# Optimization experiments

Measured on AMD Instinct MI355X. Metric: run time of the kernel, lower is better.

The kernel has to match this reference:

```python
import jax, jax.numpy as jnp
import numpy as np
import math

HEAD_DIM = 128
THETA = 10000.0
MASK_VAL = -10000.0


def _rope(x, cos, sin):
    # x: (B, S, D); cos/sin: (S, D//2). Pairs (even, odd) rotated as complex.
    xr = x.reshape(*x.shape[:-1], -1, 2)
    xe, xo = xr[..., 0], xr[..., 1]
    oe = xe * cos - xo * sin
    oo = xe * sin + xo * cos
    return jnp.stack([oe, oo], axis=-1).reshape(x.shape)


def setup_inputs() -> dict:
    key = jax.random.key(0)
    B, S, D = 8, 4096, HEAD_DIM
    qkv = jax.random.normal(key, (B, S, 3 * D), dtype=jnp.float32)
    return {"qkv": qkv}


def reference(qkv):
    B, S, threeD = qkv.shape
    D = threeD // 3
    qkv = qkv.reshape(B, S, 3, D)
    q, k, v = qkv[:, :, 0], qkv[:, :, 1], qkv[:, :, 2]

    # precompute_freqs_cis: outer(t, 1/theta^(2i/d)) -> cos/sin (S, D//2)
    inv_freq = 1.0 / (THETA ** (jnp.arange(0, D, 2, dtype=jnp.float32) / D))
    freqs = jnp.arange(S, dtype=jnp.float32)[:, None] * inv_freq[None, :]
    cos, sin = jnp.cos(freqs), jnp.sin(freqs)
    q = _rope(q, cos, sin)
    k = _rope(k, cos, sin)

    scale = 1.0 / math.sqrt(D)
    scores = jnp.einsum('btd,bsd->bts', q, k) * scale  # (B, S, S)
    causal_mask = jnp.triu(jnp.full((S, S), MASK_VAL, dtype=scores.dtype), 1)
    attn = jax.nn.softmax(scores + causal_mask, axis=-1)
    out = jnp.einsum('bts,bsd->btd', attn, v)  # (B, S, D)
    return out
```

## Files before the change

kernel.cpp:

```cpp
#include <hip/hip_runtime.h>
#include <math.h>

typedef _Float16 half8 __attribute__((ext_vector_type(8)));
typedef float floatx4 __attribute__((ext_vector_type(4)));
typedef float floatx2 __attribute__((ext_vector_type(2)));

#define B_ 8
#define S_ 4096
#define SCALE_L2E 0.12751743008389106f
#define MASK_L2E  -14426.950408889634f
#define L2_10K_OVER_128 0.10381025296522975f

#define PLD2 40
#define KW  136
#define VW  24
#define OSTLD 136
#define SLOTS_PER_B 576
#define NW 8
#define POOL_HALFS (16384 + NW * 2 * 16 * PLD2)

__device__ __forceinline__ int chunk_prefix(int qt32) {
    int g = qt32 >> 4;
    return qt32 + 8 * g * (g - 1) + (qt32 - (g << 4)) * g;
}

__device__ __forceinline__ void glds16(const _Float16* src, _Float16* dst) {
    __builtin_amdgcn_global_load_lds((const __attribute__((address_space(1))) void*)src,
                                     (__attribute__((address_space(3))) void*)dst, 16, 0, 0);
}

__global__ __launch_bounds__(256) void prep_kernel(const float* __restrict__ qkv,
                                                   _Float16* __restrict__ Qh,
                                                   _Float16* __restrict__ Kp,
                                                   _Float16* __restrict__ Vp) {
    __shared__ __align__(16) _Float16 Kl[16][KW];
    __shared__ __align__(16) _Float16 Vt[128][VW];
    const int tid = threadIdx.x;
    const int b   = blockIdx.y;
    const int s0  = blockIdx.x * 16;

#pragma unroll
    for (int it = 0; it < 4; ++it) {
        int idx = tid + it * 256;
        int i = idx & 63, sr = idx >> 6, s = s0 + sr;
        const float* base = qkv + ((size_t)(b * S_ + s)) * 384 + 2 * i;
        floatx2 q2 = *(const floatx2*)base;
        floatx2 k2 = *(const floatx2*)(base + 128);
        float inv = exp2f(-(float)(2 * i) * L2_10K_OVER_128);
        float ang = (float)s * inv;
        float sn, cs;
        __sincosf(ang, &sn, &cs);
        size_t oq = ((size_t)(b * S_ + s)) * 128 + 2 * i;
        Qh[oq]     = (_Float16)((q2[0] * cs - q2[1] * sn) * SCALE_L2E);
        Qh[oq + 1] = (_Float16)((q2[0] * sn + q2[1] * cs) * SCALE_L2E);
        Kl[sr][2 * i]     = (_Float16)(k2[0] * cs - k2[1] * sn);
        Kl[sr][2 * i + 1] = (_Float16)(k2[0] * sn + k2[1] * cs);
    }
#pragma unroll
    for (int it = 0; it < 2; ++it) {
        int idx = tid + it * 256;
        int c = idx & 31, sr = idx >> 5;
        floatx4 v = *(const floatx4*)(qkv + ((size_t)(b * S_ + s0 + sr)) * 384 + 256 + c * 4);
#pragma unroll
        for (int j = 0; j < 4; ++j) Vt[c * 4 + j][sr] = (_Float16)v[j];
    }
    __syncthreads();

    {
        int c = tid >> 6, lane = tid & 63;
        int quad = lane >> 4, n = lane & 15;
        half8 val = *(const half8*)&Kl[n][c * 32 + quad * 8];
        int s16 = s0 >> 4;
        *(half8*)(Kp + (((size_t)(b * 256 + s16) * 4 + c) * 64 + lane) * 8) = val;
    }
    {
        int kt = s0 >> 6, c2 = (s0 >> 5) & 1, qp = (s0 >> 4) & 1;
        int nt = tid >> 5, lq = (tid >> 4) & 1, n = tid & 15;
        int quad = qp * 2 + lq;
        int lane = quad * 16 + n;
        half8 val = *(const half8*)&Vt[nt * 16 + n][lq * 8];
        *(half8*)(Vp + ((((size_t)(b * 64 + kt) * 2 + c2) * 8 + nt) * 64 + lane) * 8) = val;
    }
}

__global__ __launch_bounds__(512) void attn_part_kernel(const _Float16* __restrict__ Qh,
                                                        const _Float16* __restrict__ Kp,
                                                        const _Float16* __restrict__ Vp,
                                                        _Float16* __restrict__ Ppart,
                                                        float* __restrict__ Lpart) {
    __shared__ __align__(16) _Float16 POOL[POOL_HALFS];

    const int tid  = threadIdx.x;
    const int w    = tid >> 6;
    const int lane = tid & 63;
    const int quad = lane >> 4;
    const int l16  = lane & 15;
    const int b     = blockIdx.x & 7;
    const int chunk = blockIdx.x >> 3;
    const int c0    = chunk * 8;

    const int qt32_top  = 127 - blockIdx.y * 8;
    const int ktmax_blk = (qt32_top * 32 + 31) >> 6;
    if (c0 > ktmax_blk) return;
    const int kend_blk  = min(ktmax_blk, c0 + 7);

    const int qt32   = qt32_top - w;
    const int qr0    = qt32 * 32;
    const int kt_max = (qr0 + 31) >> 6;
    const bool has_work = (c0 <= kt_max);
    const int kend   = min(kt_max, c0 + 7);
    const int slot   = b * SLOTS_PER_B + chunk_prefix(qt32) + chunk;
    _Float16* Pw = POOL + 16384 + w * (2 * 16 * PLD2);

    half8 aq[2][4];
#pragma unroll
    for (int tile = 0; tile < 2; ++tile) {
        const _Float16* Qb = Qh + ((size_t)(b * S_) + qr0 + tile * 16 + l16) * 128;
#pragma unroll
        for (int c = 0; c < 4; ++c) aq[tile][c] = *(const half8*)(Qb + c * 32 + quad * 8);
    }

    floatx4 o[2][8];
#pragma unroll
    for (int tile = 0; tile < 2; ++tile)
#pragma unroll
        for (int i = 0; i < 8; ++i) o[tile][i] = (floatx4){0.f, 0.f, 0.f, 0.f};
    float rsum[2][4] = {{0.f, 0.f, 0.f, 0.f}, {0.f, 0.f, 0.f, 0.f}};

    const _Float16* Kb = Kp + (size_t)b * 524288;
    const _Float16* Vb = Vp + (size_t)b * 524288;

    const int ht0    = 2 * c0;
    const int ht_end = 2 * kend_blk + 1;

    {
        const _Float16* ks = Kb + (size_t)ht0 * 4096 + w * 512 + lane * 8;
        const _Float16* vs = Vb + (size_t)ht0 * 4096 + w * 512 + lane * 8;
        glds16(ks, POOL + w * 512);
        glds16(vs, POOL + 4096 + w * 512);
    }

    for (int ht = ht0; ht <= ht_end; ++ht) {
        const int buf = ht & 1;
        if (ht < ht_end) {
            const _Float16* ks = Kb + (size_t)(ht + 1) * 4096 + w * 512 + lane * 8;
            const _Float16* vs = Vb + (size_t)(ht + 1) * 4096 + w * 512 + lane * 8;
            _Float16* kd = POOL + (buf ^ 1) * 8192 + w * 512;
            glds16(ks, kd);
            glds16(vs, kd + 4096);
            asm volatile("s_waitcnt vmcnt(2)" ::: "memory");
        } else {
            asm volatile("s_waitcnt vmcnt(0)" ::: "memory");
        }
        __builtin_amdgcn_s_barrier();

        const int kt = ht >> 1, h = ht & 1;
        if (has_work && kt <= kend) {
            const _Float16* Klds = POOL + buf * 8192;
            const _Float16* Vlds = Klds + 4096;

            floatx4 s4[2][2];
#pragma unroll
            for (int tl = 0; tl < 2; ++tl) {
                half8 bk[4];
#pragma unroll
                for (int c = 0; c < 4; ++c)
                    bk[c] = *(const half8*)&Klds[((tl * 4 + c) * 64 + lane) * 8];
                floatx4 a0 = (floatx4){0.f, 0.f, 0.f, 0.f};
                floatx4 a1 = (floatx4){0.f, 0.f, 0.f, 0.f};
                __builtin_amdgcn_s_setprio(1);
#pragma unroll
                for (int c = 0; c < 4; ++c) {
                    a0 = __builtin_amdgcn_mfma_f32_16x16x32_f16(aq[0][c], bk[c], a0, 0, 0, 0);
                    a1 = __builtin_amdgcn_mfma_f32_16x16x32_f16(aq[1][c], bk[c], a1, 0, 0, 0);
                }
                __builtin_amdgcn_s_setprio(0);
                s4[0][tl] = a0; s4[1][tl] = a1;
            }

            if (kt == kt_max) {
#pragma unroll
                for (int tile = 0; tile < 2; ++tile)
#pragma unroll
                    for (int tl = 0; tl < 2; ++tl)
#pragma unroll
                        for (int r = 0; r < 4; ++r) {
                            int kcol = kt * 64 + h * 32 + tl * 16 + l16;
                            int qr   = qr0 + tile * 16 + quad * 4 + r;
                            if (kcol > qr) s4[tile][tl][r] += MASK_L2E;
                        }
            }

#pragma unroll
            for (int tile = 0; tile < 2; ++tile)
#pragma unroll
                for (int tl = 0; tl < 2; ++tl)
#pragma unroll
                    for (int r = 0; r < 4; ++r) {
                        float p = __builtin_amdgcn_exp2f(s4[tile][tl][r]);
                        rsum[tile][r] += p;
                        Pw[tile * (16 * PLD2) + (quad * 4 + r) * PLD2 + tl * 16 + l16] = (_Float16)p;
                    }

            {
                half8 vf[8];
#pragma unroll
                for (int nt = 0; nt < 8; ++nt)
                    vf[nt] = *(const half8*)&Vlds[(nt * 64 + lane) * 8];
#pragma unroll
                for (int tile = 0; tile < 2; ++tile) {
                    half8 ap = *(const half8*)&Pw[tile * (16 * PLD2) + l16 * PLD2 + quad * 8];
                    __builtin_amdgcn_s_setprio(1);
#pragma unroll
                    for (int nt = 0; nt < 8; ++nt)
                        o[tile][nt] = __builtin_amdgcn_mfma_f32_16x16x32_f16(ap, vf[nt], o[tile][nt], 0, 0, 0);
                    __builtin_amdgcn_s_setprio(0);
                }
            }
        }
        asm volatile("" ::: "memory");
        __builtin_amdgcn_s_barrier();
    }

    if (!has_work) return;

#pragma unroll
    for (int off = 1; off <= 8; off <<= 1)
#pragma unroll
        for (int tile = 0; tile < 2; ++tile)
#pragma unroll
            for (int r = 0; r < 4; ++r)
                rsum[tile][r] += __shfl_xor(rsum[tile][r], off, 64);
    if (l16 == 0) {
#pragma unroll
        for (int tile = 0; tile < 2; ++tile)
#pragma unroll
            for (int r = 0; r < 4; ++r)
                Lpart[(size_t)slot * 32 + tile * 16 + quad * 4 + r] = rsum[tile][r];
    }

    asm volatile("" ::: "memory");
    _Float16* Ost = POOL + w * (POOL_HALFS / NW);
    _Float16* pp = Ppart + (size_t)slot * 4096;
#pragma unroll
    for (int tile = 0; tile < 2; ++tile) {
#pragma unroll
        for (int nt = 0; nt < 8; ++nt)
#pragma unroll
            for (int r = 0; r < 4; ++r)
                Ost[(quad * 4 + r) * OSTLD + nt * 16 + l16] = (_Float16)o[tile][nt][r];
#pragma unroll
        for (int i = 0; i < 4; ++i) {
            int idx = lane + i * 64;
            half8 v = *(const half8*)&Ost[(idx >> 4) * OSTLD + (idx & 15) * 8];
            *(half8*)(pp + ((size_t)tile * 256 + idx) * 8) = v;
        }
    }
}

__global__ __launch_bounds__(256) void reduce_kernel(const _Float16* __restrict__ Ppart,
                                                     const float* __restrict__ Lpart,
                                                     float* __restrict__ out) {
    const int bid  = blockIdx.x;
    const int b    = bid >> 7;
    const int qt32 = bid & 127;
    const int qr0  = qt32 * 32;
    const int nch  = (((qr0 + 31) >> 6) >> 3) + 1;
    const int slot0 = b * SLOTS_PER_B + chunk_prefix(qt32);
    const _Float16* pp = Ppart + (size_t)slot0 * 4096;
    const float* lp = Lpart + (size_t)slot0 * 32;
    const int tid = threadIdx.x;

#pragma unroll
    for (int j = 0; j < 2; ++j) {
        int idx = tid + j * 256;
        int row = idx >> 4;
        float acc[8] = {0.f, 0.f, 0.f, 0.f, 0.f, 0.f, 0.f, 0.f};
        float l = 0.f;
        for (int c = 0; c < nch; ++c) {
            half8 v = *(const half8*)(pp + (size_t)c * 4096 + (size_t)idx * 8);
#pragma unroll
            for (int k = 0; k < 8; ++k) acc[k] += (float)v[k];
            l += lp[c * 32 + row];
        }
        float inv = 1.0f / l;
        float* ob = out + ((size_t)(b * S_) + qr0) * 128 + (size_t)idx * 8;
        floatx4 o0 = (floatx4){acc[0] * inv, acc[1] * inv, acc[2] * inv, acc[3] * inv};
        floatx4 o1 = (floatx4){acc[4] * inv, acc[5] * inv, acc[6] * inv, acc[7] * inv};
        *(floatx4*)ob = o0;
        *(floatx4*)(ob + 4) = o1;
    }
}

#define PLD 72
__global__ __launch_bounds__(64) void attn_atomic_kernel(const _Float16* __restrict__ Qh,
                                                         const _Float16* __restrict__ Kp,
                                                         const _Float16* __restrict__ Vp,
                                                         float* __restrict__ out,
                                                         float* __restrict__ Lg) {
    __shared__ __align__(16) _Float16 Pl[2][16 * PLD];
    const int lane = threadIdx.x, quad = lane >> 4, l16 = lane & 15;
    const int b = blockIdx.x & 7, chunk = blockIdx.x >> 3;
    const int qt = 255 - blockIdx.y, qr0 = qt * 16;
    const int kt_max = qt >> 2, c0 = chunk * 8;
    if (c0 > kt_max) return;
    const int kend = min(kt_max, c0 + 7);
    const _Float16* Qb = Qh + ((size_t)(b * S_) + qr0 + l16) * 128;
    half8 aq[4];
#pragma unroll
    for (int c = 0; c < 4; ++c) aq[c] = *(const half8*)(Qb + c * 32 + quad * 8);
    floatx4 o[8];
#pragma unroll
    for (int i = 0; i < 8; ++i) o[i] = (floatx4){0.f, 0.f, 0.f, 0.f};
    float rsum[4] = {0.f, 0.f, 0.f, 0.f};
    const _Float16* Kb = Kp + (size_t)b * 524288;
    const _Float16* Vb = Vp + (size_t)b * 524288;
    for (int kt = c0; kt <= kend; ++kt) {
        half8 vf[2][8];
#pragma unroll
        for (int c2 = 0; c2 < 2; ++c2)
#pragma unroll
            for (int nt = 0; nt < 8; ++nt)
                vf[c2][nt] = *(const half8*)(Vb + (((size_t)(kt * 2 + c2) * 8 + nt) * 64 + lane) * 8);
        floatx4 s4[4];
#pragma unroll
        for (int t = 0; t < 4; ++t) {
            const _Float16* kp = Kb + ((size_t)((kt * 4 + t) * 4) * 64 + lane) * 8;
            floatx4 acc = (floatx4){0.f, 0.f, 0.f, 0.f};
#pragma unroll
            for (int c = 0; c < 4; ++c) {
                half8 bk = *(const half8*)(kp + c * 512);
                acc = __builtin_amdgcn_mfma_f32_16x16x32_f16(aq[c], bk, acc, 0, 0, 0);
            }
            s4[t] = acc;
        }
        if (kt == kt_max) {
#pragma unroll
            for (int t = 0; t < 4; ++t)
#pragma unroll
                for (int r = 0; r < 4; ++r) {
                    int kcol = kt * 64 + t * 16 + l16;
                    int qr = qr0 + quad * 4 + r;
                    if (kcol > qr) s4[t][r] += MASK_L2E;
                }
        }
        const int buf = kt & 1;
#pragma unroll
        for (int t = 0; t < 4; ++t)
#pragma unroll
            for (int r = 0; r < 4; ++r) {
                float p = __builtin_amdgcn_exp2f(s4[t][r]);
                rsum[r] += p;
                Pl[buf][(quad * 4 + r) * PLD + t * 16 + l16] = (_Float16)p;
            }
#pragma unroll
        for (int c2 = 0; c2 < 2; ++c2) {
            half8 ap = *(const half8*)&Pl[buf][l16 * PLD + c2 * 32 + quad * 8];
#pragma unroll
            for (int nt = 0; nt < 8; ++nt)
                o[nt] = __builtin_amdgcn_mfma_f32_16x16x32_f16(ap, vf[c2][nt], o[nt], 0, 0, 0);
        }
    }
#pragma unroll
    for (int off = 1; off <= 8; off <<= 1)
#pragma unroll
        for (int r = 0; r < 4; ++r)
            rsum[r] += __shfl_xor(rsum[r], off, 64);
    if (l16 == 0) {
#pragma unroll
        for (int r = 0; r < 4; ++r)
            atomicAdd(&Lg[(size_t)(b * S_) + qr0 + quad * 4 + r], rsum[r]);
    }
    float* ob = out + ((size_t)(b * S_) + qr0) * 128;
#pragma unroll
    for (int nt = 0; nt < 8; ++nt)
#pragma unroll
        for (int r = 0; r < 4; ++r)
            atomicAdd(&ob[(quad * 4 + r) * 128 + nt * 16 + l16], o[nt][r]);
}

__global__ __launch_bounds__(256) void norm_kernel(float* __restrict__ out,
                                                   const float* __restrict__ Lg) {
    int i = blockIdx.x * 256 + threadIdx.x;
    int row = i >> 5;
    floatx4 v = *(floatx4*)(out + (size_t)i * 4);
    float inv = 1.0f / Lg[row];
    v[0] *= inv; v[1] *= inv; v[2] *= inv; v[3] *= inv;
    *(floatx4*)(out + (size_t)i * 4) = v;
}

extern "C" void kernel_launch(void* const* d_in, const int* in_sizes, int n_in,
                              void* d_out, int out_size, void* d_ws, size_t ws_size,
                              hipStream_t stream) {
    const float* qkv = (const float*)d_in[0];
    float* out = (float*)d_out;
    const size_t MB = 1024 * 1024;
    _Float16* Qh = (_Float16*)d_ws;
    _Float16* Kp = (_Float16*)((char*)d_ws + 8 * MB);
    _Float16* Vp = (_Float16*)((char*)d_ws + 16 * MB);

    const size_t lpart_bytes = (size_t)B_ * SLOTS_PER_B * 32 * sizeof(float);
    const size_t ppart_bytes = (size_t)B_ * SLOTS_PER_B * 4096 * sizeof(_Float16);
    const size_t need = 25 * MB + ppart_bytes;

    prep_kernel<<<dim3(256, B_), dim3(256), 0, stream>>>(qkv, Qh, Kp, Vp);

    if (ws_size >= need) {
        float*    Lpart = (float*)((char*)d_ws + 24 * MB);
        _Float16* Ppart = (_Float16*)((char*)d_ws + 25 * MB);
        (void)lpart_bytes;
        attn_part_kernel<<<dim3(64, 16), dim3(512), 0, stream>>>(Qh, Kp, Vp, Ppart, Lpart);
        reduce_kernel<<<dim3(1024), dim3(256), 0, stream>>>(Ppart, Lpart, out);
    } else {
        float* Lg = (float*)((char*)d_ws + 24 * MB);
        hipMemsetAsync(out, 0, (size_t)B_ * S_ * 128 * sizeof(float), stream);
        hipMemsetAsync(Lg, 0, (size_t)B_ * S_ * sizeof(float), stream);
        attn_atomic_kernel<<<dim3(64, 256), dim3(64), 0, stream>>>(Qh, Kp, Vp, out, Lg);
        norm_kernel<<<dim3(4096), dim3(256), 0, stream>>>(out, Lg);
    }
}
```

Baseline: 164.7 us.

## Triple-buffer K/V staging and drop the per-iteration trailing barrier

Switches the K/V shared-memory staging from double to triple buffering, prefetching two half-tiles ahead. The next load is issued after the top barrier, which makes the second barrier at the end of each loop iteration unnecessary, so it is removed. The change also hoists the V fragment loads ahead of the softmax exponentials and drops the s_setprio hints around the MFMA blocks. The aim is to halve barrier synchronisation and better hide global-to-LDS latency, at the cost of more LDS per block, which may reduce occupancy.

```diff
diff --git a/kernel.cpp b/kernel.cpp
--- a/kernel.cpp
+++ b/kernel.cpp
@@ -17,7 +17,10 @@
 #define OSTLD 136
 #define SLOTS_PER_B 576
 #define NW 8
-#define POOL_HALFS (16384 + NW * 2 * 16 * PLD2)
+#define KVBUF 8192
+#define NBUF 3
+#define POFF (NBUF * KVBUF)
+#define POOL_HALFS (POFF + NW * 2 * 16 * PLD2)
 
 __device__ __forceinline__ int chunk_prefix(int qt32) {
     int g = qt32 >> 4;
@@ -110,7 +113,7 @@
     const bool has_work = (c0 <= kt_max);
     const int kend   = min(kt_max, c0 + 7);
     const int slot   = b * SLOTS_PER_B + chunk_prefix(qt32) + chunk;
-    _Float16* Pw = POOL + 16384 + w * (2 * 16 * PLD2);
+    _Float16* Pw = POOL + POFF + w * (2 * 16 * PLD2);
 
     half8 aq[2][4];
 #pragma unroll
@@ -133,30 +136,30 @@
     const int ht0    = 2 * c0;
     const int ht_end = 2 * kend_blk + 1;
 
-    {
-        const _Float16* ks = Kb + (size_t)ht0 * 4096 + w * 512 + lane * 8;
-        const _Float16* vs = Vb + (size_t)ht0 * 4096 + w * 512 + lane * 8;
-        glds16(ks, POOL + w * 512);
-        glds16(vs, POOL + 4096 + w * 512);
-    }
+#define STAGE(ht_)                                                                \
+    do {                                                                          \
+        const _Float16* ks_ = Kb + (size_t)(ht_) * 4096 + w * 512 + lane * 8;     \
+        const _Float16* vs_ = Vb + (size_t)(ht_) * 4096 + w * 512 + lane * 8;     \
+        _Float16* d_ = POOL + ((ht_) % NBUF) * KVBUF + w * 512;                   \
+        glds16(ks_, d_);                                                          \
+        glds16(vs_, d_ + 4096);                                                   \
+    } while (0)
+
+    STAGE(ht0);
+    STAGE(ht0 + 1);
 
     for (int ht = ht0; ht <= ht_end; ++ht) {
-        const int buf = ht & 1;
         if (ht < ht_end) {
-            const _Float16* ks = Kb + (size_t)(ht + 1) * 4096 + w * 512 + lane * 8;
-            const _Float16* vs = Vb + (size_t)(ht + 1) * 4096 + w * 512 + lane * 8;
-            _Float16* kd = POOL + (buf ^ 1) * 8192 + w * 512;
-            glds16(ks, kd);
-            glds16(vs, kd + 4096);
             asm volatile("s_waitcnt vmcnt(2)" ::: "memory");
         } else {
             asm volatile("s_waitcnt vmcnt(0)" ::: "memory");
         }
         __builtin_amdgcn_s_barrier();
+        if (ht + 2 <= ht_end) STAGE(ht + 2);
 
         const int kt = ht >> 1, h = ht & 1;
         if (has_work && kt <= kend) {
-            const _Float16* Klds = POOL + buf * 8192;
+            const _Float16* Klds = POOL + (ht % NBUF) * KVBUF;
             const _Float16* Vlds = Klds + 4096;
 
             floatx4 s4[2][2];
@@ -168,15 +171,18 @@
                     bk[c] = *(const half8*)&Klds[((tl * 4 + c) * 64 + lane) * 8];
                 floatx4 a0 = (floatx4){0.f, 0.f, 0.f, 0.f};
                 floatx4 a1 = (floatx4){0.f, 0.f, 0.f, 0.f};
-                __builtin_amdgcn_s_setprio(1);
 #pragma unroll
                 for (int c = 0; c < 4; ++c) {
                     a0 = __builtin_amdgcn_mfma_f32_16x16x32_f16(aq[0][c], bk[c], a0, 0, 0, 0);
                     a1 = __builtin_amdgcn_mfma_f32_16x16x32_f16(aq[1][c], bk[c], a1, 0, 0, 0);
                 }
-                __builtin_amdgcn_s_setprio(0);
                 s4[0][tl] = a0; s4[1][tl] = a1;
             }
+
+            half8 vf[8];
+#pragma unroll
+            for (int nt = 0; nt < 8; ++nt)
+                vf[nt] = *(const half8*)&Vlds[(nt * 64 + lane) * 8];
 
             if (kt == kt_max) {
 #pragma unroll
@@ -202,25 +208,18 @@
                         Pw[tile * (16 * PLD2) + (quad * 4 + r) * PLD2 + tl * 16 + l16] = (_Float16)p;
                     }
 
-            {
-                half8 vf[8];
+#pragma unroll
+            for (int tile = 0; tile < 2; ++tile) {
+                half8 ap = *(const half8*)&Pw[tile * (16 * PLD2) + l16 * PLD2 + quad * 8];
 #pragma unroll
                 for (int nt = 0; nt < 8; ++nt)
-                    vf[nt] = *(const half8*)&Vlds[(nt * 64 + lane) * 8];
-#pragma unroll
-                for (int tile = 0; tile < 2; ++tile) {
-                    half8 ap = *(const half8*)&Pw[tile * (16 * PLD2) + l16 * PLD2 + quad * 8];
-                    __builtin_amdgcn_s_setprio(1);
-#pragma unroll
-                    for (int nt = 0; nt < 8; ++nt)
-                        o[tile][nt] = __builtin_amdgcn_mfma_f32_16x16x32_f16(ap, vf[nt], o[tile][nt], 0, 0, 0);
-                    __builtin_amdgcn_s_setprio(0);
-                }
+                    o[tile][nt] = __builtin_amdgcn_mfma_f32_16x16x32_f16(ap, vf[nt], o[tile][nt], 0, 0, 0);
             }
         }
-        asm volatile("" ::: "memory");
-        __builtin_amdgcn_s_barrier();
-    }
+    }
+#undef STAGE
+
+    __builtin_amdgcn_s_barrier();
 
     if (!has_work) return;
 
@@ -239,7 +238,6 @@
                 Lpart[(size_t)slot * 32 + tile * 16 + quad * 4 + r] = rsum[tile][r];
     }
 
-    asm volatile("" ::: "memory");
     _Float16* Ost = POOL + w * (POOL_HALFS / NW);
     _Float16* pp = Ppart + (size_t)slot * 4096;
 #pragma unroll
```

New measurement: 165.0 us. Within noise of the previous version (+0.2%).
